# Optimization experiments

Hardware: AMD Instinct MI355X
Metric: run time of the kernel (lower is better)

## Reference

```python
import jax, jax.numpy as jnp
import numpy as np

# Dimensions
N = 16384    # batch of tree nodes (original code is batch-1 per node; math is identical per row)
WD, TD, RD = 300, 50, 50   # word / tag / rel feature dims
H = 512      # mlp_com_hid_dim
M = 512      # mem_dim == mlp_com_out_dim (required by additive gate combination)
G = 5        # gates: [i, f_down, f_left, o, u]
W_SCALE = 0.05


def setup_inputs() -> dict:
    key = jax.random.key(0)
    ks = jax.random.split(key, 32)
    def rn(i, shape, s=1.0):
        return jax.random.normal(ks[i], shape, dtype=jnp.float32) * s
    return dict(
        word=rn(0, (N, WD)), tag=rn(1, (N, TD)), rel=rn(2, (N, RD)),
        k=rn(3, (N, M)), q=rn(4, (N, M)), h_prev=rn(5, (N, M)), c_prev=rn(6, (N, M)),
        # com_MLP params, stacked over the 5 gates
        W_word=rn(7, (G, H, WD), W_SCALE), b_word=rn(8, (G, H), W_SCALE),
        W_tag=rn(9, (G, H, TD), W_SCALE),  b_tag=rn(10, (G, H), W_SCALE),
        W_rel=rn(11, (G, H, RD), W_SCALE), b_rel=rn(12, (G, H), W_SCALE),
        W_hid=rn(13, (G, H, H), W_SCALE),  b_hid=rn(14, (G, H), W_SCALE),
        W_last=rn(15, (G, M, H), W_SCALE), b_last=rn(16, (G, M), W_SCALE),
        # per-gate Linear(mem_dim, mem_dim) applied to h_prev and k
        W_hp=rn(17, (G, M, M), W_SCALE), b_hp=rn(18, (G, M), W_SCALE),
        W_k=rn(19, (G, M, M), W_SCALE),  b_k=rn(20, (G, M), W_SCALE),
    )


def reference(word, tag, rel, k, q, h_prev, c_prev,
              W_word, b_word, W_tag, b_tag, W_rel, b_rel,
              W_hid, b_hid, W_last, b_last,
              W_hp, b_hp, W_k, b_k):
    # com_MLP for all 5 gates at once (eval mode: dropout = identity)
    h0 = jnp.tanh(jnp.einsum('nw,ghw->gnh', word, W_word)
                  + jnp.einsum('nt,ght->gnh', tag, W_tag)
                  + jnp.einsum('nr,ghr->gnh', rel, W_rel)
                  + (b_word + b_tag + b_rel)[:, None, :])            # [G,N,H]
    h1 = jnp.tanh(jnp.einsum('gnh,gkh->gnk', h0, W_hid) + b_hid[:, None, :])   # hidden layer
    m = jnp.tanh(jnp.einsum('gnh,gmh->gnm', h1, W_last) + b_last[:, None, :])  # [G,N,M]
    # gate pre-activations: mlp + W_h h_prev + W_k k (with biases)
    pre = (m
           + jnp.einsum('nm,gom->gno', h_prev, W_hp) + b_hp[:, None, :]
           + jnp.einsum('nm,gom->gno', k, W_k) + b_k[:, None, :])    # [G,N,M]
    i_g    = jax.nn.sigmoid(pre[0])
    f_down = jax.nn.sigmoid(pre[1])
    f_left = jax.nn.sigmoid(pre[2])
    o_g    = jax.nn.sigmoid(pre[3])
    u_g    = jnp.tanh(pre[4])
    c = i_g * u_g + f_down * q + f_left * c_prev
    h = o_g * jnp.tanh(c)
    return (h, c)
```

## Files before the change

### kernel.cpp

```cpp
#include <hip/hip_runtime.h>
#include <math.h>

#define NROWS 16384
#define GATES 5
#define HDIM 512
#define KPAD 416

using bf16x8 = __attribute__((ext_vector_type(8))) short;
using f32x4  = __attribute__((ext_vector_type(4))) float;

__device__ inline float b2f(unsigned short s) {
  unsigned int u = ((unsigned int)s) << 16;
  return __builtin_bit_cast(float, u);
}
__device__ inline unsigned short f2b(float f) {
  unsigned int u = __builtin_bit_cast(unsigned int, f);
  u += 0x7fffu + ((u >> 16) & 1u);
  return (unsigned short)(u >> 16);
}

__device__ inline float fast_sigmoid(float x) {
  float t = __builtin_amdgcn_exp2f(-1.4426950408889634f * x);
  return __builtin_amdgcn_rcpf(1.0f + t);
}
__device__ inline float fast_tanh(float x) {
  float t = __builtin_amdgcn_exp2f(2.8853900817779268f * x);
  return 1.0f - 2.0f * __builtin_amdgcn_rcpf(1.0f + t);
}

__device__ inline void gload_lds16(const unsigned short* g, unsigned short* l) {
  __builtin_amdgcn_global_load_lds(
      (const __attribute__((address_space(1))) unsigned int*)(g),
      (__attribute__((address_space(3))) unsigned int*)(l), 16, 0, 0);
}

__device__ inline void cfence() { asm volatile("" ::: "memory"); }
__device__ inline void hard_barrier() {
  cfence();
  __builtin_amdgcn_s_barrier();
  cfence();
}


__global__ void pack_x(const float* __restrict__ word,
                       const float* __restrict__ tag,
                       const float* __restrict__ rel,
                       unsigned short* __restrict__ xcat) {
  int idx = blockIdx.x * 256 + threadIdx.x;
  if (idx >= NROWS * KPAD) return;
  int n = idx / KPAD, c = idx % KPAD;
  float v = 0.f;
  if (c < 300)      v = word[n * 300 + c];
  else if (c < 350) v = tag[n * 50 + (c - 300)];
  else if (c < 400) v = rel[n * 50 + (c - 350)];
  xcat[idx] = f2b(v);
}

__global__ void pack_w(const float* __restrict__ Ww,
                       const float* __restrict__ Wt,
                       const float* __restrict__ Wr,
                       unsigned short* __restrict__ Wcat) {
  int idx = blockIdx.x * 256 + threadIdx.x;
  if (idx >= GATES * HDIM * KPAD) return;
  int gh = idx / KPAD;
  int c = idx % KPAD;
  float v = 0.f;
  if (c < 300)      v = Ww[gh * 300 + c];
  else if (c < 350) v = Wt[gh * 50 + (c - 300)];
  else if (c < 400) v = Wr[gh * 50 + (c - 350)];
  Wcat[idx] = f2b(v);
}

__global__ void cvt_w4(const float* __restrict__ a, const float* __restrict__ b,
                       const float* __restrict__ c, const float* __restrict__ d,
                       unsigned short* oa, unsigned short* ob,
                       unsigned short* oc, unsigned short* od) {
  const float* in; unsigned short* out;
  switch (blockIdx.y) {
    case 0: in = a; out = oa; break;
    case 1: in = b; out = ob; break;
    case 2: in = c; out = oc; break;
    default: in = d; out = od; break;
  }
  int i = (blockIdx.x * 256 + threadIdx.x) * 4;
  float4 v = *(const float4*)(in + i);
  ushort4 o;
  o.x = f2b(v.x); o.y = f2b(v.y); o.z = f2b(v.z); o.w = f2b(v.w);
  *(ushort4*)(out + i) = o;
}

__global__ void cvt_x2(const float* __restrict__ a, const float* __restrict__ b,
                       unsigned short* oa, unsigned short* ob) {
  const float* in = blockIdx.y ? b : a;
  unsigned short* out = blockIdx.y ? ob : oa;
  int i = (blockIdx.x * 256 + threadIdx.x) * 4;
  float4 v = *(const float4*)(in + i);
  ushort4 o;
  o.x = f2b(v.x); o.y = f2b(v.y); o.z = f2b(v.z); o.w = f2b(v.w);
  *(ushort4*)(out + i) = o;
}

__global__ void pack_bias(const float* __restrict__ bw, const float* __restrict__ bt,
                          const float* __restrict__ br, const float* __restrict__ bh,
                          const float* __restrict__ bl, const float* __restrict__ bhp,
                          const float* __restrict__ bk,
                          float* bias0, float* bias1, float* bias2, float* biasD) {
  int i = blockIdx.x * 256 + threadIdx.x;
  if (i < GATES * HDIM) {
    bias0[i] = bw[i] + bt[i] + br[i];
    bias1[i] = bh[i];
    bias2[i] = bl[i];
    biasD[i] = bhp[i] + bk[i];
  }
}



__global__ __launch_bounds__(512, 2) void gemm_mlp(
    const unsigned short* __restrict__ A1,
    const unsigned short* __restrict__ W1,
    const float* __restrict__ bias,
    unsigned short* __restrict__ Out,
    int aPerGate, int S, int ld)
{
  __shared__ __align__(16) unsigned short smem[36864];
  unsigned short* Ab0 = smem;
  unsigned short* Bb0 = smem + 24576;
  unsigned short* eps = smem;

  const int bid = (int)blockIdx.x;
  const int swz = (bid & 7) * 160 + (bid >> 3);
  const int col = swz % 20, rowt = swz / 20;
  const int row0  = rowt * 256;
  const int gcol0 = col * 128;
  const int g = gcol0 >> 9;
  const size_t aslab = aPerGate ? (size_t)g * NROWS * ld : 0;

  const int t = threadIdx.x;
  const int wid = t >> 6, l = t & 63;
  const int wrow = (wid >> 2) * 128;
  const int wcol = (wid & 3) * 32;
  const int fr = l & 15, q = l >> 4;

  f32x4 acc[8][2];
#pragma unroll
  for (int mi = 0; mi < 8; ++mi)
#pragma unroll
    for (int ni = 0; ni < 2; ++ni)
      acc[mi][ni] = (f32x4){0.f, 0.f, 0.f, 0.f};

  auto stage = [&](int c, int buf) {
    const int kloc = c * 32;
    const int rb = t >> 2;
#pragma unroll
    for (int j = 0; j < 2; ++j) {
      const int r = j * 128 + rb;
      const int sgj = ((t & 3) ^ ((r >> 1) & 3)) * 8;
      gload_lds16(A1 + aslab + (size_t)(row0 + r) * ld + kloc + sgj, &Ab0[buf * 8192 + j * 4096 + t * 8]);
    }
    const int sg = ((t & 3) ^ ((rb >> 1) & 3)) * 8;
    gload_lds16(W1 + (size_t)(gcol0 + rb) * ld + kloc + sg, &Bb0[buf * 4096 + t * 8]);
  };

  cfence();
  stage(0, 0);
  if (S > 1) stage(1, 1);
  cfence();

  for (int s = 0; s < S; ++s) {
    const int buf = s % 3;
    if (s + 2 < S) {
      stage(s + 2, (s + 2) % 3);
      asm volatile("s_waitcnt vmcnt(6)" ::: "memory");
    } else if (s + 1 < S) {
      asm volatile("s_waitcnt vmcnt(3)" ::: "memory");
    } else {
      asm volatile("s_waitcnt vmcnt(0)" ::: "memory");
    }
    hard_barrier();

    bf16x8 bq[2];
#pragma unroll
    for (int ni = 0; ni < 2; ++ni) {
      const int r = wcol + ni * 16 + fr;
      bq[ni] = *reinterpret_cast<const bf16x8*>(&Bb0[buf * 4096 + r * 32 + ((q ^ ((r >> 1) & 3)) * 8)]);
    }
#pragma unroll
    for (int p = 0; p < 2; ++p) {
      bf16x8 af[4];
#pragma unroll
      for (int mi = 0; mi < 4; ++mi) {
        const int r = wrow + (p * 4 + mi) * 16 + fr;
        af[mi] = *reinterpret_cast<const bf16x8*>(&Ab0[buf * 8192 + r * 32 + ((q ^ ((r >> 1) & 3)) * 8)]);
      }
      __builtin_amdgcn_s_setprio(1);
#pragma unroll
      for (int mi = 0; mi < 4; ++mi)
#pragma unroll
        for (int ni = 0; ni < 2; ++ni)
          acc[p * 4 + mi][ni] = __builtin_amdgcn_mfma_f32_16x16x32_bf16(af[mi], bq[ni], acc[p * 4 + mi][ni], 0, 0, 0);
      __builtin_amdgcn_s_setprio(0);
    }
    hard_barrier();
  }

  const size_t NM = (size_t)NROWS * HDIM;
  unsigned short* outg = Out + (size_t)g * NM;
  const int colbase = gcol0 & 511;
  float bv[2];
#pragma unroll
  for (int ni = 0; ni < 2; ++ni)
    bv[ni] = bias[g * HDIM + colbase + wcol + ni * 16 + fr];

#pragma unroll
  for (int h = 0; h < 4; ++h) {
    hard_barrier();
    if ((wid >> 2) == (h >> 1)) {
      const int mib = (h & 1) * 4;
#pragma unroll
      for (int mi2 = 0; mi2 < 4; ++mi2)
#pragma unroll
        for (int ni = 0; ni < 2; ++ni)
#pragma unroll
          for (int j = 0; j < 4; ++j)
            eps[(mi2 * 16 + q * 4 + j) * 132 + wcol + ni * 16 + fr] =
                f2b(fast_tanh(acc[mib + mi2][ni][j] + bv[ni]));
    }
    asm volatile("s_waitcnt lgkmcnt(0)" ::: "memory");
    hard_barrier();
#pragma unroll
    for (int v = 0; v < 2; ++v) {
      const int c  = v * 512 + t;
      const int rl = c >> 4;
      const int cc = (c & 15) * 8;
      const int gr = row0 + h * 64 + rl;
      bf16x8 pv = *reinterpret_cast<const bf16x8*>(&eps[rl * 132 + cc]);
      *reinterpret_cast<bf16x8*>(&outg[(size_t)gr * HDIM + colbase + cc]) = pv;
    }
  }
}


__global__ __launch_bounds__(512, 2) void gemm_cd(
    const unsigned short* __restrict__ H1,
    const unsigned short* __restrict__ Hp,
    const unsigned short* __restrict__ Kb,
    const unsigned short* __restrict__ Wl,
    const unsigned short* __restrict__ Whp,
    const unsigned short* __restrict__ Wk,
    const float* __restrict__ bias2, const float* __restrict__ biasD,
    unsigned short* __restrict__ Out)
{
  __shared__ __align__(16) unsigned short smem[36864];
  unsigned short* Ab0 = smem;
  unsigned short* Bb0 = smem + 24576;
  unsigned short* eps = smem;

  const int bid = (int)blockIdx.x;
  const int swz = (bid & 7) * 160 + (bid >> 3);
  const int col = swz % 20, rowt = swz / 20;
  const int row0  = rowt * 256;
  const int gcol0 = col * 128;
  const int g = gcol0 >> 9;

  const int t = threadIdx.x;
  const int wid = t >> 6, l = t & 63;
  const int wrow = (wid >> 2) * 128;
  const int wcol = (wid & 3) * 32;
  const int fr = l & 15, q = l >> 4;

  f32x4 acc[8][2];
#pragma unroll
  for (int mi = 0; mi < 8; ++mi)
#pragma unroll
    for (int ni = 0; ni < 2; ++ni)
      acc[mi][ni] = (f32x4){0.f, 0.f, 0.f, 0.f};

  auto stageG = [&](const unsigned short* Asrc, const unsigned short* Wsrc,
                    int kloc, int buf) {
    const int rb = t >> 2;
#pragma unroll
    for (int j = 0; j < 2; ++j) {
      const int r = j * 128 + rb;
      const int sgj = ((t & 3) ^ ((r >> 1) & 3)) * 8;
      gload_lds16(Asrc + (size_t)(row0 + r) * HDIM + kloc + sgj, &Ab0[buf * 8192 + j * 4096 + t * 8]);
    }
    const int sg = ((t & 3) ^ ((rb >> 1) & 3)) * 8;
    gload_lds16(Wsrc + (size_t)(gcol0 + rb) * HDIM + kloc + sg, &Bb0[buf * 4096 + t * 8]);
  };

  auto runloop = [&](int S, auto srcpick) {
    cfence();
    { auto s0 = srcpick(0); stageG(s0.a, s0.w, s0.k, 0); }
    if (S > 1) { auto s1 = srcpick(1); stageG(s1.a, s1.w, s1.k, 1); }
    cfence();
    for (int s = 0; s < S; ++s) {
      const int buf = s % 3;
      if (s + 2 < S) {
        auto sn = srcpick(s + 2);
        stageG(sn.a, sn.w, sn.k, (s + 2) % 3);
        asm volatile("s_waitcnt vmcnt(6)" ::: "memory");
      } else if (s + 1 < S) {
        asm volatile("s_waitcnt vmcnt(3)" ::: "memory");
      } else {
        asm volatile("s_waitcnt vmcnt(0)" ::: "memory");
      }
      hard_barrier();

      bf16x8 bq[2];
#pragma unroll
      for (int ni = 0; ni < 2; ++ni) {
        const int r = wcol + ni * 16 + fr;
        bq[ni] = *reinterpret_cast<const bf16x8*>(&Bb0[buf * 4096 + r * 32 + ((q ^ ((r >> 1) & 3)) * 8)]);
      }
#pragma unroll
      for (int p = 0; p < 2; ++p) {
        bf16x8 af[4];
#pragma unroll
        for (int mi = 0; mi < 4; ++mi) {
          const int r = wrow + (p * 4 + mi) * 16 + fr;
          af[mi] = *reinterpret_cast<const bf16x8*>(&Ab0[buf * 8192 + r * 32 + ((q ^ ((r >> 1) & 3)) * 8)]);
        }
        __builtin_amdgcn_s_setprio(1);
#pragma unroll
        for (int mi = 0; mi < 4; ++mi)
#pragma unroll
          for (int ni = 0; ni < 2; ++ni)
            acc[p * 4 + mi][ni] = __builtin_amdgcn_mfma_f32_16x16x32_bf16(af[mi], bq[ni], acc[p * 4 + mi][ni], 0, 0, 0);
        __builtin_amdgcn_s_setprio(0);
      }
      hard_barrier();
    }
  };

  struct Src { const unsigned short* a; const unsigned short* w; int k; };
  const size_t NM = (size_t)NROWS * HDIM;

  const unsigned short* h1g = H1 + (size_t)g * NM;
  runloop(16, [&](int c) -> Src { return {h1g, Wl, c * 32}; });

  const int colbase = gcol0 & 511;
#pragma unroll
  for (int ni = 0; ni < 2; ++ni) {
    const float b2 = bias2[g * HDIM + colbase + wcol + ni * 16 + fr];
    const float bD = biasD[g * HDIM + colbase + wcol + ni * 16 + fr];
#pragma unroll
    for (int mi = 0; mi < 8; ++mi)
#pragma unroll
      for (int j = 0; j < 4; ++j)
        acc[mi][ni][j] = fast_tanh(acc[mi][ni][j] + b2) + bD;
  }

  runloop(32, [&](int c) -> Src {
    return (c < 16) ? Src{Hp, Whp, c * 32} : Src{Kb, Wk, (c - 16) * 32};
  });

  unsigned short* outg = Out + (size_t)g * NM;
#pragma unroll
  for (int h = 0; h < 4; ++h) {
    hard_barrier();
    if ((wid >> 2) == (h >> 1)) {
      const int mib = (h & 1) * 4;
#pragma unroll
      for (int mi2 = 0; mi2 < 4; ++mi2)
#pragma unroll
        for (int ni = 0; ni < 2; ++ni)
#pragma unroll
          for (int j = 0; j < 4; ++j) {
            float v = acc[mib + mi2][ni][j];
            v = (g < 4) ? fast_sigmoid(v) : fast_tanh(v);
            eps[(mi2 * 16 + q * 4 + j) * 132 + wcol + ni * 16 + fr] = f2b(v);
          }
    }
    asm volatile("s_waitcnt lgkmcnt(0)" ::: "memory");
    hard_barrier();
#pragma unroll
    for (int v = 0; v < 2; ++v) {
      const int c  = v * 512 + t;
      const int rl = c >> 4;
      const int cc = (c & 15) * 8;
      const int gr = row0 + h * 64 + rl;
      bf16x8 pv = *reinterpret_cast<const bf16x8*>(&eps[rl * 132 + cc]);
      *reinterpret_cast<bf16x8*>(&outg[(size_t)gr * HDIM + colbase + cc]) = pv;
    }
  }
}


__device__ inline float exb(const uint4& v, int j) {
  unsigned int wd = ((const unsigned int*)&v)[j >> 1];
  return b2f((unsigned short)(wd >> ((j & 1) * 16)));
}

__global__ void combine(const unsigned short* __restrict__ gates,
                        const float* __restrict__ q,
                        const float* __restrict__ cp,
                        float* __restrict__ out) {
  const size_t NM = (size_t)NROWS * HDIM;
  size_t i8 = ((size_t)blockIdx.x * 256 + threadIdx.x) * 8;
  if (i8 >= NM) return;
  uint4 gi = *(const uint4*)(gates + 0 * NM + i8);
  uint4 gf = *(const uint4*)(gates + 1 * NM + i8);
  uint4 gl = *(const uint4*)(gates + 2 * NM + i8);
  uint4 go = *(const uint4*)(gates + 3 * NM + i8);
  uint4 gu = *(const uint4*)(gates + 4 * NM + i8);
  float4 q0 = *(const float4*)(q + i8);
  float4 q1 = *(const float4*)(q + i8 + 4);
  float4 p0 = *(const float4*)(cp + i8);
  float4 p1 = *(const float4*)(cp + i8 + 4);
  float qv[8] = {q0.x, q0.y, q0.z, q0.w, q1.x, q1.y, q1.z, q1.w};
  float pv[8] = {p0.x, p0.y, p0.z, p0.w, p1.x, p1.y, p1.z, p1.w};
  float hv[8], cv[8];
#pragma unroll
  for (int j = 0; j < 8; ++j) {
    float c = exb(gi, j) * exb(gu, j) + exb(gf, j) * qv[j] + exb(gl, j) * pv[j];
    hv[j] = exb(go, j) * fast_tanh(c);
    cv[j] = c;
  }
  *(float4*)(out + i8)      = make_float4(hv[0], hv[1], hv[2], hv[3]);
  *(float4*)(out + i8 + 4)  = make_float4(hv[4], hv[5], hv[6], hv[7]);
  *(float4*)(out + NM + i8)     = make_float4(cv[0], cv[1], cv[2], cv[3]);
  *(float4*)(out + NM + i8 + 4) = make_float4(cv[4], cv[5], cv[6], cv[7]);
}


extern "C" void kernel_launch(void* const* d_in, const int* in_sizes, int n_in,
                              void* d_out, int out_size, void* d_ws, size_t ws_size,
                              hipStream_t stream) {
  const float* word  = (const float*)d_in[0];
  const float* tag   = (const float*)d_in[1];
  const float* rel   = (const float*)d_in[2];
  const float* kin   = (const float*)d_in[3];
  const float* qin   = (const float*)d_in[4];
  const float* hprev = (const float*)d_in[5];
  const float* cprev = (const float*)d_in[6];
  const float* Ww    = (const float*)d_in[7];
  const float* bw    = (const float*)d_in[8];
  const float* Wt    = (const float*)d_in[9];
  const float* bt    = (const float*)d_in[10];
  const float* Wr    = (const float*)d_in[11];
  const float* br    = (const float*)d_in[12];
  const float* Wh    = (const float*)d_in[13];
  const float* bh    = (const float*)d_in[14];
  const float* Wl    = (const float*)d_in[15];
  const float* bl    = (const float*)d_in[16];
  const float* Whp   = (const float*)d_in[17];
  const float* bhp   = (const float*)d_in[18];
  const float* Wk    = (const float*)d_in[19];
  const float* bk    = (const float*)d_in[20];

  char* ws = (char*)d_ws;
  unsigned short* xcat   = (unsigned short*)(ws);
  unsigned short* Wcat   = (unsigned short*)(ws + 13631488);
  unsigned short* Whb    = (unsigned short*)(ws + 15761408);
  unsigned short* Wlb    = (unsigned short*)(ws + 18382848);
  unsigned short* Whpb   = (unsigned short*)(ws + 21004288);
  unsigned short* Wkb    = (unsigned short*)(ws + 23625728);
  unsigned short* hprevb = (unsigned short*)(ws + 26247168);
  unsigned short* kb16   = (unsigned short*)(ws + 43024384);
  float* bias0           = (float*)(ws + 59801600);
  float* bias1           = (float*)(ws + 59811840);
  float* bias2           = (float*)(ws + 59822080);
  float* biasD           = (float*)(ws + 59832320);
  unsigned short* bufA   = (unsigned short*)(ws + 59842560);
  unsigned short* bufB   = (unsigned short*)(ws + 143728640);

  pack_x<<<26624, 256, 0, stream>>>(word, tag, rel, xcat);
  pack_w<<<4160, 256, 0, stream>>>(Ww, Wt, Wr, Wcat);
  cvt_w4<<<dim3(1280, 4), 256, 0, stream>>>(Wh, Wl, Whp, Wk, Whb, Wlb, Whpb, Wkb);
  cvt_x2<<<dim3(8192, 2), 256, 0, stream>>>(hprev, kin, hprevb, kb16);
  pack_bias<<<10, 256, 0, stream>>>(bw, bt, br, bh, bl, bhp, bk, bias0, bias1, bias2, biasD);

  const int grid = (NROWS / 256) * ((GATES * HDIM) / 128);
  gemm_mlp<<<grid, 512, 0, stream>>>(xcat, Wcat, bias0, bufA, 0, 13, KPAD);
  gemm_mlp<<<grid, 512, 0, stream>>>(bufA, Whb, bias1, bufB, 1, 16, HDIM);
  gemm_cd<<<grid, 512, 0, stream>>>(bufB, hprevb, kb16, Wlb, Whpb, Wkb,
                                    bias2, biasD, bufA);
  combine<<<4096, 256, 0, stream>>>(bufA, qin, cprev, (float*)d_out);
}
```

Before: 358.7 us.

## Merge preprocessing kernels and use one barrier per K-step in GEMM loops

Five small conversion and packing kernels become two combined launches, one for activations and one for weights and biases, which cuts kernel launch overhead and tail gaps. In both GEMM main loops the second per-iteration barrier is removed. Each iteration now waits for its own stage (vmcnt 3), syncs once, and then issues the prefetch for s+2 into the buffer that was read two steps earlier, relying on triple buffering for safety. This halves the barriers per K-step, at the cost of issuing the prefetch later and thinner margins on reuse of the rotating buffers.

```diff
diff --git a/kernel.cpp b/kernel.cpp
--- a/kernel.cpp
+++ b/kernel.cpp
@@ -42,75 +42,81 @@
 }
 
 
-__global__ void pack_x(const float* __restrict__ word,
-                       const float* __restrict__ tag,
-                       const float* __restrict__ rel,
-                       unsigned short* __restrict__ xcat) {
-  int idx = blockIdx.x * 256 + threadIdx.x;
-  if (idx >= NROWS * KPAD) return;
-  int n = idx / KPAD, c = idx % KPAD;
-  float v = 0.f;
-  if (c < 300)      v = word[n * 300 + c];
-  else if (c < 350) v = tag[n * 50 + (c - 300)];
-  else if (c < 400) v = rel[n * 50 + (c - 350)];
-  xcat[idx] = f2b(v);
-}
-
-__global__ void pack_w(const float* __restrict__ Ww,
-                       const float* __restrict__ Wt,
-                       const float* __restrict__ Wr,
-                       unsigned short* __restrict__ Wcat) {
-  int idx = blockIdx.x * 256 + threadIdx.x;
-  if (idx >= GATES * HDIM * KPAD) return;
-  int gh = idx / KPAD;
-  int c = idx % KPAD;
-  float v = 0.f;
-  if (c < 300)      v = Ww[gh * 300 + c];
-  else if (c < 350) v = Wt[gh * 50 + (c - 300)];
-  else if (c < 400) v = Wr[gh * 50 + (c - 350)];
-  Wcat[idx] = f2b(v);
-}
-
-__global__ void cvt_w4(const float* __restrict__ a, const float* __restrict__ b,
-                       const float* __restrict__ c, const float* __restrict__ d,
-                       unsigned short* oa, unsigned short* ob,
-                       unsigned short* oc, unsigned short* od) {
-  const float* in; unsigned short* out;
-  switch (blockIdx.y) {
-    case 0: in = a; out = oa; break;
-    case 1: in = b; out = ob; break;
-    case 2: in = c; out = oc; break;
-    default: in = d; out = od; break;
-  }
-  int i = (blockIdx.x * 256 + threadIdx.x) * 4;
-  float4 v = *(const float4*)(in + i);
-  ushort4 o;
-  o.x = f2b(v.x); o.y = f2b(v.y); o.z = f2b(v.z); o.w = f2b(v.w);
-  *(ushort4*)(out + i) = o;
-}
-
-__global__ void cvt_x2(const float* __restrict__ a, const float* __restrict__ b,
-                       unsigned short* oa, unsigned short* ob) {
-  const float* in = blockIdx.y ? b : a;
-  unsigned short* out = blockIdx.y ? ob : oa;
-  int i = (blockIdx.x * 256 + threadIdx.x) * 4;
-  float4 v = *(const float4*)(in + i);
-  ushort4 o;
-  o.x = f2b(v.x); o.y = f2b(v.y); o.z = f2b(v.z); o.w = f2b(v.w);
-  *(ushort4*)(out + i) = o;
-}
-
-__global__ void pack_bias(const float* __restrict__ bw, const float* __restrict__ bt,
-                          const float* __restrict__ br, const float* __restrict__ bh,
-                          const float* __restrict__ bl, const float* __restrict__ bhp,
-                          const float* __restrict__ bk,
-                          float* bias0, float* bias1, float* bias2, float* biasD) {
-  int i = blockIdx.x * 256 + threadIdx.x;
-  if (i < GATES * HDIM) {
-    bias0[i] = bw[i] + bt[i] + br[i];
-    bias1[i] = bh[i];
-    bias2[i] = bl[i];
-    biasD[i] = bhp[i] + bk[i];
+__global__ void aux_inputs(const float* __restrict__ word,
+                           const float* __restrict__ tag,
+                           const float* __restrict__ rel,
+                           const float* __restrict__ hprev,
+                           const float* __restrict__ kin,
+                           unsigned short* __restrict__ xcat,
+                           unsigned short* __restrict__ hprevb,
+                           unsigned short* __restrict__ kb) {
+  int b = blockIdx.x;
+  if (b < 26624) {
+    int idx = b * 256 + threadIdx.x;
+    if (idx >= NROWS * KPAD) return;
+    int n = idx / KPAD, c = idx % KPAD;
+    float v = 0.f;
+    if (c < 300)      v = word[n * 300 + c];
+    else if (c < 350) v = tag[n * 50 + (c - 300)];
+    else if (c < 400) v = rel[n * 50 + (c - 350)];
+    xcat[idx] = f2b(v);
+  } else {
+    int b2 = b - 26624;
+    const float* in = (b2 < 8192) ? hprev : kin;
+    unsigned short* out = (b2 < 8192) ? hprevb : kb;
+    int i = (((b2 & 8191) * 256) + threadIdx.x) * 4;
+    float4 v = *(const float4*)(in + i);
+    ushort4 o;
+    o.x = f2b(v.x); o.y = f2b(v.y); o.z = f2b(v.z); o.w = f2b(v.w);
+    *(ushort4*)(out + i) = o;
+  }
+}
+
+__global__ void aux_weights(const float* __restrict__ Ww, const float* __restrict__ Wt,
+                            const float* __restrict__ Wr,
+                            const float* __restrict__ Wh, const float* __restrict__ Wl,
+                            const float* __restrict__ Whp, const float* __restrict__ Wk,
+                            const float* __restrict__ bw, const float* __restrict__ bt,
+                            const float* __restrict__ br, const float* __restrict__ bh,
+                            const float* __restrict__ bl, const float* __restrict__ bhp,
+                            const float* __restrict__ bk,
+                            unsigned short* __restrict__ Wcat,
+                            unsigned short* __restrict__ Whb, unsigned short* __restrict__ Wlb,
+                            unsigned short* __restrict__ Whpb, unsigned short* __restrict__ Wkb,
+                            float* bias0, float* bias1, float* bias2, float* biasD) {
+  int b = blockIdx.x;
+  if (b < 4160) {
+    int idx = b * 256 + threadIdx.x;
+    if (idx >= GATES * HDIM * KPAD) return;
+    int gh = idx / KPAD, c = idx % KPAD;
+    float v = 0.f;
+    if (c < 300)      v = Ww[gh * 300 + c];
+    else if (c < 350) v = Wt[gh * 50 + (c - 300)];
+    else if (c < 400) v = Wr[gh * 50 + (c - 350)];
+    Wcat[idx] = f2b(v);
+  } else if (b < 9280) {
+    int b2 = b - 4160;
+    int sel = b2 / 1280;
+    const float* in; unsigned short* out;
+    switch (sel) {
+      case 0: in = Wh;  out = Whb;  break;
+      case 1: in = Wl;  out = Wlb;  break;
+      case 2: in = Whp; out = Whpb; break;
+      default: in = Wk; out = Wkb;  break;
+    }
+    int i = (((b2 % 1280) * 256) + threadIdx.x) * 4;
+    float4 v = *(const float4*)(in + i);
+    ushort4 o;
+    o.x = f2b(v.x); o.y = f2b(v.y); o.z = f2b(v.z); o.w = f2b(v.w);
+    *(ushort4*)(out + i) = o;
+  } else {
+    int i = (b - 9280) * 256 + threadIdx.x;
+    if (i < GATES * HDIM) {
+      bias0[i] = bw[i] + bt[i] + br[i];
+      bias1[i] = bh[i];
+      bias2[i] = bl[i];
+      biasD[i] = bhp[i] + bk[i];
+    }
   }
 }
 
@@ -169,15 +175,10 @@
 
   for (int s = 0; s < S; ++s) {
     const int buf = s % 3;
-    if (s + 2 < S) {
-      stage(s + 2, (s + 2) % 3);
-      asm volatile("s_waitcnt vmcnt(6)" ::: "memory");
-    } else if (s + 1 < S) {
-      asm volatile("s_waitcnt vmcnt(3)" ::: "memory");
-    } else {
-      asm volatile("s_waitcnt vmcnt(0)" ::: "memory");
-    }
-    hard_barrier();
+    if (s < S - 1) asm volatile("s_waitcnt vmcnt(3)" ::: "memory");
+    else           asm volatile("s_waitcnt vmcnt(0)" ::: "memory");
+    hard_barrier();
+    if (s + 2 < S) stage(s + 2, (s + 2) % 3);
 
     bf16x8 bq[2];
 #pragma unroll
@@ -201,8 +202,8 @@
           acc[p * 4 + mi][ni] = __builtin_amdgcn_mfma_f32_16x16x32_bf16(af[mi], bq[ni], acc[p * 4 + mi][ni], 0, 0, 0);
       __builtin_amdgcn_s_setprio(0);
     }
-    hard_barrier();
-  }
+  }
+  hard_barrier();
 
   const size_t NM = (size_t)NROWS * HDIM;
   unsigned short* outg = Out + (size_t)g * NM;
@@ -296,16 +297,13 @@
     cfence();
     for (int s = 0; s < S; ++s) {
       const int buf = s % 3;
+      if (s < S - 1) asm volatile("s_waitcnt vmcnt(3)" ::: "memory");
+      else           asm volatile("s_waitcnt vmcnt(0)" ::: "memory");
+      hard_barrier();
       if (s + 2 < S) {
         auto sn = srcpick(s + 2);
         stageG(sn.a, sn.w, sn.k, (s + 2) % 3);
-        asm volatile("s_waitcnt vmcnt(6)" ::: "memory");
-      } else if (s + 1 < S) {
-        asm volatile("s_waitcnt vmcnt(3)" ::: "memory");
-      } else {
-        asm volatile("s_waitcnt vmcnt(0)" ::: "memory");
       }
-      hard_barrier();
 
       bf16x8 bq[2];
 #pragma unroll
@@ -329,8 +327,8 @@
             acc[p * 4 + mi][ni] = __builtin_amdgcn_mfma_f32_16x16x32_bf16(af[mi], bq[ni], acc[p * 4 + mi][ni], 0, 0, 0);
         __builtin_amdgcn_s_setprio(0);
       }
-      hard_barrier();
-    }
+    }
+    hard_barrier();
   };
 
   struct Src { const unsigned short* a; const unsigned short* w; int k; };
@@ -465,11 +463,12 @@
   unsigned short* bufA   = (unsigned short*)(ws + 59842560);
   unsigned short* bufB   = (unsigned short*)(ws + 143728640);
 
-  pack_x<<<26624, 256, 0, stream>>>(word, tag, rel, xcat);
-  pack_w<<<4160, 256, 0, stream>>>(Ww, Wt, Wr, Wcat);
-  cvt_w4<<<dim3(1280, 4), 256, 0, stream>>>(Wh, Wl, Whp, Wk, Whb, Wlb, Whpb, Wkb);
-  cvt_x2<<<dim3(8192, 2), 256, 0, stream>>>(hprev, kin, hprevb, kb16);
-  pack_bias<<<10, 256, 0, stream>>>(bw, bt, br, bh, bl, bhp, bk, bias0, bias1, bias2, biasD);
+  aux_inputs<<<43008, 256, 0, stream>>>(word, tag, rel, hprev, kin,
+                                        xcat, hprevb, kb16);
+  aux_weights<<<9290, 256, 0, stream>>>(Ww, Wt, Wr, Wh, Wl, Whp, Wk,
+                                        bw, bt, br, bh, bl, bhp, bk,
+                                        Wcat, Whb, Wlb, Whpb, Wkb,
+                                        bias0, bias1, bias2, biasD);
 
   const int grid = (NROWS / 256) * ((GATES * HDIM) / 128);
   gemm_mlp<<<grid, 512, 0, stream>>>(xcat, Wcat, bias0, bufA, 0, 13, KPAD);
```

Result: faster. 345.8 us, median of 3 (-3.6%).
